# Optimization experiments

Measured on AMD Instinct MI355X. Metric: run time of the kernel, lower is better.

Reference implementation:

```python
import jax, jax.numpy as jnp
import numpy as np

N_NODES = 50000
N_EDGES = 800000
IN_C = 64
HID = 64
OUT_C = 64
N_GRAPHS = 64


def setup_inputs() -> dict:
    key = jax.random.key(0)
    ks = jax.random.split(key, 12)
    x = jax.random.normal(ks[0], (N_NODES, IN_C), dtype=jnp.float32)
    edge_index = jax.random.randint(ks[1], (2, N_EDGES), 0, N_NODES, dtype=jnp.int64)
    # sorted graph-id vector guaranteed to cover all N_GRAPHS segments
    batch = (jnp.arange(N_NODES, dtype=jnp.int64) * N_GRAPHS) // N_NODES
    s = 0.1
    W1_root = jax.random.normal(ks[2], (IN_C, HID), dtype=jnp.float32) * s
    W1_rel = jax.random.normal(ks[3], (IN_C, HID), dtype=jnp.float32) * s
    b1 = jnp.zeros((HID,), dtype=jnp.float32)
    W2_root = jax.random.normal(ks[4], (HID, OUT_C), dtype=jnp.float32) * s
    W2_rel = jax.random.normal(ks[5], (HID, OUT_C), dtype=jnp.float32) * s
    b2 = jnp.zeros((OUT_C,), dtype=jnp.float32)
    fc1_w = jax.random.normal(ks[6], (OUT_C, 8), dtype=jnp.float32) * s
    fc1_b = jnp.zeros((8,), dtype=jnp.float32)
    fc2_w = jax.random.normal(ks[7], (8, 2), dtype=jnp.float32) * s
    fc2_b = jnp.zeros((2,), dtype=jnp.float32)
    return {
        "x": x, "edge_index": edge_index, "batch": batch,
        "W1_root": W1_root, "W1_rel": W1_rel, "b1": b1,
        "W2_root": W2_root, "W2_rel": W2_rel, "b2": b2,
        "fc1_w": fc1_w, "fc1_b": fc1_b, "fc2_w": fc2_w, "fc2_b": fc2_b,
    }


def _graph_conv(h, src, dst, W_root, W_rel, b, n_nodes):
    # PyG GraphConv (aggr='add'): out_i = W_root h_i + W_rel * sum_{j->i} h_j + b
    agg = jax.ops.segment_sum(h[src], dst, num_segments=n_nodes)
    return h @ W_root + agg @ W_rel + b


def reference(x, edge_index, batch, W1_root, W1_rel, b1,
              W2_root, W2_rel, b2, fc1_w, fc1_b, fc2_w, fc2_b):
    n = x.shape[0]
    src, dst = edge_index[0], edge_index[1]
    h = jax.nn.relu(_graph_conv(x, src, dst, W1_root, W1_rel, b1, n))
    h = jax.nn.relu(_graph_conv(h, src, dst, W2_root, W2_rel, b2, n))
    # mid = softmax over first 8 feature columns (split(8,1)[0])
    mid = jax.nn.softmax(h[:, :8], axis=1)
    z = jax.nn.relu(h @ fc1_w + fc1_b)
    z = jax.nn.relu(z @ fc2_w + fc2_b)
    pooled = jax.ops.segment_max(z, batch, num_segments=N_GRAPHS)  # global_max_pool
    out = jax.nn.softmax(pooled, axis=1)
    return (mid, out)
```

## Files before the change

kernel.cpp:

```cpp
#include <hip/hip_runtime.h>
#include <hip/hip_fp16.h>

typedef _Float16 f16_t;
typedef _Float16 f16x8 __attribute__((ext_vector_type(8)));
typedef float f32x4 __attribute__((ext_vector_type(4)));

#define N_NODES 50000
#define N_EDGES 800000
#define C 64
#define N_GRAPHS 64

#define NBKT 782
#define BKT_CAP 1536
#define HS_BLOCKS 256
#define HS_EPB (N_EDGES / HS_BLOCKS)
#define CAST_BLKS 1563
#define CUR_STRIDE 16

#define OFF_CUR    0u
#define OFF_POOLED 51200u
#define OFF_DONE   51712u
#define OFF_EPK    52224u
#define OFF_XH     4857088u
#define OFF_H1H    11257344u
#define OFF_WT1    17657600u
#define OFF_WT2    17673984u

__device__ __forceinline__ unsigned pack2h(float x, float y) {
    __half2 h = __floats2half2_rn(x, y);
    return *reinterpret_cast<unsigned*>(&h);
}

__global__ __launch_bounds__(256) void init_cast_wcast_kernel(
        const float* __restrict__ x, f16_t* __restrict__ xh,
        const float* __restrict__ W1r, const float* __restrict__ W1l, f16_t* __restrict__ Wt1,
        const float* __restrict__ W2r, const float* __restrict__ W2l, f16_t* __restrict__ Wt2,
        int* __restrict__ cur, unsigned int* __restrict__ pooled,
        unsigned int* __restrict__ done_cnt) {
    __shared__ float w0[64 * 64];
    __shared__ float w1[64 * 64];
    const int blk = blockIdx.x;
    const int t = threadIdx.x;
    if (blk < CAST_BLKS) {
        if (blk == 0) {
            for (int i = t; i < NBKT * CUR_STRIDE; i += 256) cur[i] = 0;
            if (t < N_GRAPHS * 2) pooled[t] = 0u;
            if (t == 0) *done_cnt = 0u;
        }
        const int i = blk * 256 + t;
        if (i < N_NODES * C / 8) {
            const float4* p = (const float4*)(x + (size_t)i * 8);
            float4 a = p[0], b = p[1];
            uint4 w;
            w.x = pack2h(a.x, a.y);
            w.y = pack2h(a.z, a.w);
            w.z = pack2h(b.x, b.y);
            w.w = pack2h(b.z, b.w);
            *(uint4*)(xh + (size_t)i * 8) = w;
        }
    } else {
        const int which = blk - CAST_BLKS;
        const float* Wr = which ? W2r : W1r;
        const float* Wl = which ? W2l : W1l;
        f16_t* Wt = which ? Wt2 : Wt1;
        for (int i = t * 4; i < 4096; i += 1024) {
            *(float4*)&w0[i] = *(const float4*)&Wr[i];
            *(float4*)&w1[i] = *(const float4*)&Wl[i];
        }
        __syncthreads();
        const int n = t >> 2, q = t & 3;
        for (int kk = q * 32; kk < q * 32 + 32; kk++) {
            float v = (kk < 64) ? w0[kk * 64 + n] : w1[(kk - 64) * 64 + n];
            Wt[n * 128 + kk] = (f16_t)v;
        }
    }
}

__global__ __launch_bounds__(256) void hist_scatter_kernel(const int* __restrict__ src,
                                                           const int* __restrict__ dst,
                                                           int* __restrict__ cur,
                                                           int* __restrict__ epk) {
    __shared__ int h[NBKT];
    __shared__ int base_s[NBKT];
    const int t = threadIdx.x;
    const int blk = blockIdx.x;
    for (int i = t; i < NBKT; i += 256) h[i] = 0;
    __syncthreads();
    const int beg = blk * HS_EPB;
    for (int i = beg + t; i < beg + HS_EPB; i += 256)
        atomicAdd(&h[dst[i] >> 6], 1);
    __syncthreads();
    for (int b = t; b < NBKT; b += 256) {
        int hv = h[b];
        int old = hv ? atomicAdd(&cur[b * CUR_STRIDE], hv) : 0;
        base_s[b] = b * BKT_CAP + old;
        h[b] = 0;
    }
    __syncthreads();
    for (int i = beg + t; i < beg + HS_EPB; i += 256) {
        int d = dst[i];
        int b = d >> 6;
        int off = atomicAdd(&h[b], 1);
        int pos = base_s[b] + off;
        if (pos < (b + 1) * BKT_CAP)
            epk[pos] = src[i] | ((d & 63) << 16);
    }
}

__device__ __forceinline__ void agg_stage_mfma(
        const f16_t* __restrict__ Hsrc,
        const int* __restrict__ epk_blk, int n_edges,
        const f16_t* __restrict__ Wt, const float* __restrict__ bias,
        f16_t* Als, f16_t* Wls, int* eb, int* cnt, int* beg,
        int row0, int t, f32x4& acc, int& ncol, int& outrow0) {
    const int cr = t >> 4, cj = t & 15;
    int gxr = row0 + cr; if (gxr > N_NODES - 1) gxr = N_NODES - 1;
    uint2 xv = *(const uint2*)(Hsrc + (size_t)gxr * 64 + cj * 4);
    uint4 wvv = *(const uint4*)(Wt + cr * 128 + cj * 8);
    if (t < 64) cnt[t] = 0;
    __syncthreads();
    int pk0 = (t < n_edges) ? epk_blk[t] : -1;
    int pk1 = (t + 1024 < n_edges) ? epk_blk[t + 1024] : -1;
    if (pk0 >= 0) atomicAdd(&cnt[pk0 >> 16], 1);
    if (pk1 >= 0) atomicAdd(&cnt[pk1 >> 16], 1);
    __syncthreads();
    if (t < 64) {
        int v = cnt[t];
        int ex = v;
        #pragma unroll
        for (int d = 1; d < 64; d <<= 1) {
            int o = __shfl_up(ex, d);
            if (t >= d) ex += o;
        }
        beg[t] = ex - v;
        cnt[t] = ex - v;
    }
    __syncthreads();
    if (pk0 >= 0) eb[atomicAdd(&cnt[pk0 >> 16], 1)] = pk0 & 0xFFFF;
    if (pk1 >= 0) eb[atomicAdd(&cnt[pk1 >> 16], 1)] = pk1 & 0xFFFF;
    __syncthreads();
    const int wv = t >> 6, lane = t & 63;
    const int slot = lane >> 4, j = lane & 15;
    const uint2* hw = (const uint2*)Hsrc;
    #pragma unroll
    for (int i = 0; i < 4; i++) {
        const int dl = wv * 4 + i;
        const int b0 = beg[dl], e1 = cnt[dl];
        float s0 = 0.f, s1 = 0.f, s2 = 0.f, s3 = 0.f;
        int e = b0;
        for (; e + 16 <= e1; e += 16) {
            int i0 = eb[e + slot];
            int i1 = eb[e + 4 + slot];
            int i2 = eb[e + 8 + slot];
            int i3 = eb[e + 12 + slot];
            uint2 u0 = hw[(size_t)i0 * 16 + j];
            uint2 u1 = hw[(size_t)i1 * 16 + j];
            uint2 u2 = hw[(size_t)i2 * 16 + j];
            uint2 u3 = hw[(size_t)i3 * 16 + j];
            float2 a, b;
            a = __half22float2(*(__half2*)&u0.x); b = __half22float2(*(__half2*)&u0.y);
            s0 += a.x; s1 += a.y; s2 += b.x; s3 += b.y;
            a = __half22float2(*(__half2*)&u1.x); b = __half22float2(*(__half2*)&u1.y);
            s0 += a.x; s1 += a.y; s2 += b.x; s3 += b.y;
            a = __half22float2(*(__half2*)&u2.x); b = __half22float2(*(__half2*)&u2.y);
            s0 += a.x; s1 += a.y; s2 += b.x; s3 += b.y;
            a = __half22float2(*(__half2*)&u3.x); b = __half22float2(*(__half2*)&u3.y);
            s0 += a.x; s1 += a.y; s2 += b.x; s3 += b.y;
        }
        for (; e + 4 <= e1; e += 4) {
            int i0 = eb[e + slot];
            uint2 u = hw[(size_t)i0 * 16 + j];
            float2 a = __half22float2(*(__half2*)&u.x);
            float2 b = __half22float2(*(__half2*)&u.y);
            s0 += a.x; s1 += a.y; s2 += b.x; s3 += b.y;
        }
        int rem = e1 - e;
        if (slot < rem) {
            int i0 = eb[e + slot];
            uint2 u = hw[(size_t)i0 * 16 + j];
            float2 a = __half22float2(*(__half2*)&u.x);
            float2 b = __half22float2(*(__half2*)&u.y);
            s0 += a.x; s1 += a.y; s2 += b.x; s3 += b.y;
        }
        s0 += __shfl_xor(s0, 16); s1 += __shfl_xor(s1, 16);
        s2 += __shfl_xor(s2, 16); s3 += __shfl_xor(s3, 16);
        s0 += __shfl_xor(s0, 32); s1 += __shfl_xor(s1, 32);
        s2 += __shfl_xor(s2, 32); s3 += __shfl_xor(s3, 32);
        if (slot == 0) {
            uint2 o; o.x = pack2h(s0, s1); o.y = pack2h(s2, s3);
            *(uint2*)((char*)Als + dl * 256 + ((128 + j * 8) ^ ((dl & 7) << 4))) = o;
        }
    }
    *(uint2*)((char*)Als + cr * 256 + ((cj * 8) ^ ((cr & 7) << 4))) = xv;
    *(uint4*)((char*)Wls + cr * 256 + ((cj * 16) ^ ((cr & 7) << 4))) = wvv;
    __syncthreads();
    const int lr = lane & 15, kh = lane >> 4;
    const int wr = wv >> 2, wc = wv & 3;
    const int arow = wr * 16 + lr;
    ncol = wc * 16 + lr;
    outrow0 = row0 + wr * 16 + kh * 4;
    float bv = bias[ncol];
    acc = (f32x4){bv, bv, bv, bv};
    #pragma unroll
    for (int kt = 0; kt < 4; kt++) {
        const int kb = (kt * 32 + kh * 8) * 2;
        f16x8 a = *(const f16x8*)((const char*)Als + arow * 256 + (kb ^ ((arow & 7) << 4)));
        f16x8 b = *(const f16x8*)((const char*)Wls + ncol * 256 + (kb ^ ((ncol & 7) << 4)));
        acc = __builtin_amdgcn_mfma_f32_16x16x32_f16(a, b, acc, 0, 0, 0);
    }
}

__global__ __launch_bounds__(1024) void layer1_kernel(const f16_t* __restrict__ xh,
                                                      const int* __restrict__ epk,
                                                      const int* __restrict__ cur,
                                                      const f16_t* __restrict__ Wt,
                                                      const float* __restrict__ bias,
                                                      f16_t* __restrict__ h1h) {
    __shared__ f16_t Als[64 * 128];
    __shared__ f16_t Wls[64 * 128];
    __shared__ int eb[BKT_CAP];
    __shared__ int cnt[64];
    __shared__ int beg[64];
    const int t = threadIdx.x;
    const int blk = blockIdx.x;
    const int row0 = blk * 64;
    int n = cur[blk * CUR_STRIDE]; if (n > BKT_CAP) n = BKT_CAP;
    f32x4 acc; int ncol, outrow0;
    agg_stage_mfma(xh, epk + (size_t)blk * BKT_CAP, n, Wt, bias,
                   Als, Wls, eb, cnt, beg, row0, t, acc, ncol, outrow0);
    #pragma unroll
    for (int rr = 0; rr < 4; rr++) {
        const int gm = outrow0 + rr;
        if (gm < N_NODES)
            h1h[(size_t)gm * 64 + ncol] = (f16_t)fmaxf(acc[rr], 0.f);
    }
}

__global__ __launch_bounds__(1024) void layer2_head_kernel(
        const f16_t* __restrict__ h1h,
        const int* __restrict__ epk, const int* __restrict__ cur,
        const f16_t* __restrict__ Wt, const float* __restrict__ bias,
        const int* __restrict__ batch,
        const float* __restrict__ fc1w, const float* __restrict__ fc1b,
        const float* __restrict__ fc2w, const float* __restrict__ fc2b,
        float* __restrict__ mid_out, unsigned int* __restrict__ pooled,
        unsigned int* __restrict__ done_cnt, float* __restrict__ fin_out) {
    __shared__ f16_t Als[64 * 128];
    __shared__ f16_t Wls[64 * 128];
    __shared__ int eb[BKT_CAP];
    __shared__ int cnt[64];
    __shared__ int beg[64];
    __shared__ float tile[64 * 65];
    __shared__ float w1s[512];
    __shared__ float z1s[64 * 9];
    __shared__ float b1s[8];
    __shared__ float w2s[16];
    __shared__ float b2s[2];
    __shared__ unsigned int pool_s[N_GRAPHS * 2];
    __shared__ unsigned int amLast;
    __shared__ float fin[N_GRAPHS * 2];
    const int t = threadIdx.x;
    const int blk = blockIdx.x;
    const int row0 = blk * 64;
    if (t < 512) w1s[t] = fc1w[t];
    if (t >= 512 && t < 520) b1s[t - 512] = fc1b[t - 512];
    if (t >= 520 && t < 536) w2s[t - 520] = fc2w[t - 520];
    if (t >= 536 && t < 538) b2s[t - 536] = fc2b[t - 536];
    if (t >= 544 && t < 544 + N_GRAPHS * 2) pool_s[t - 544] = 0u;
    int n = cur[blk * CUR_STRIDE]; if (n > BKT_CAP) n = BKT_CAP;
    f32x4 acc; int ncol, outrow0;
    agg_stage_mfma(h1h, epk + (size_t)blk * BKT_CAP, n, Wt, bias,
                   Als, Wls, eb, cnt, beg, row0, t, acc, ncol, outrow0);
    #pragma unroll
    for (int rr = 0; rr < 4; rr++)
        tile[(outrow0 - row0 + rr) * 65 + ncol] = fmaxf(acc[rr], 0.f);
    __syncthreads();
    const int row = t & 63, qq = t >> 6;
    const int gm = row0 + row;
    const bool valid = gm < N_NODES;
    if (qq < 4) {
        float z0 = b1s[2 * qq], z1v = b1s[2 * qq + 1];
        for (int k = 0; k < 64; k++) {
            float a = tile[row * 65 + k];
            z0  += a * w1s[k * 8 + 2 * qq];
            z1v += a * w1s[k * 8 + 2 * qq + 1];
        }
        z1s[row * 9 + 2 * qq]     = fmaxf(z0, 0.f);
        z1s[row * 9 + 2 * qq + 1] = fmaxf(z1v, 0.f);
    }
    if (qq == 4 && valid) {
        float rv[8];
        #pragma unroll
        for (int c = 0; c < 8; c++) rv[c] = tile[row * 65 + c];
        float m = rv[0];
        #pragma unroll
        for (int c = 1; c < 8; c++) m = fmaxf(m, rv[c]);
        float ex[8], s = 0.f;
        #pragma unroll
        for (int c = 0; c < 8; c++) { ex[c] = __expf(rv[c] - m); s += ex[c]; }
        float inv = 1.f / s;
        float4 v0 = {ex[0] * inv, ex[1] * inv, ex[2] * inv, ex[3] * inv};
        float4 v1 = {ex[4] * inv, ex[5] * inv, ex[6] * inv, ex[7] * inv};
        *(float4*)&mid_out[(size_t)gm * 8]     = v0;
        *(float4*)&mid_out[(size_t)gm * 8 + 4] = v1;
    }
    __syncthreads();
    if (qq == 0 && valid) {
        float z20 = b2s[0], z21 = b2s[1];
        #pragma unroll
        for (int o = 0; o < 8; o++) {
            float z = z1s[row * 9 + o];
            z20 += z * w2s[o * 2];
            z21 += z * w2s[o * 2 + 1];
        }
        z20 = fmaxf(z20, 0.f);
        z21 = fmaxf(z21, 0.f);
        int b = batch[gm];
        atomicMax(&pool_s[b * 2 + 0], __float_as_uint(z20));
        atomicMax(&pool_s[b * 2 + 1], __float_as_uint(z21));
    }
    __syncthreads();
    if (t < N_GRAPHS * 2) {
        unsigned int v = pool_s[t];
        if (v) atomicMax(&pooled[t], v);
    }
    __syncthreads();
    if (t == 0) {
        __threadfence();
        unsigned int prev = atomicAdd(done_cnt, 1u);
        amLast = (prev == gridDim.x - 1) ? 1u : 0u;
    }
    __syncthreads();
    if (amLast) {
        if (t < N_GRAPHS * 2) fin[t] = __uint_as_float(atomicMax(&pooled[t], 0u));
        __syncthreads();
        if (t < N_GRAPHS) {
            float v0 = fin[2 * t], v1 = fin[2 * t + 1];
            float m = fmaxf(v0, v1);
            float e0 = __expf(v0 - m), e1 = __expf(v1 - m);
            float s = e0 + e1;
            fin_out[2 * t]     = e0 / s;
            fin_out[2 * t + 1] = e1 / s;
        }
    }
}

extern "C" void kernel_launch(void* const* d_in, const int* in_sizes, int n_in,
                              void* d_out, int out_size, void* d_ws, size_t ws_size,
                              hipStream_t stream) {
    const float* x    = (const float*)d_in[0];
    const int*   ei   = (const int*)d_in[1];
    const int*   batch= (const int*)d_in[2];
    const float* W1r  = (const float*)d_in[3];
    const float* W1l  = (const float*)d_in[4];
    const float* b1   = (const float*)d_in[5];
    const float* W2r  = (const float*)d_in[6];
    const float* W2l  = (const float*)d_in[7];
    const float* b2   = (const float*)d_in[8];
    const float* fc1w = (const float*)d_in[9];
    const float* fc1b = (const float*)d_in[10];
    const float* fc2w = (const float*)d_in[11];
    const float* fc2b = (const float*)d_in[12];

    const int* src = ei;
    const int* dst = ei + N_EDGES;

    char* ws = (char*)d_ws;
    int*    cur    = (int*)(ws + OFF_CUR);
    unsigned int* pooled   = (unsigned int*)(ws + OFF_POOLED);
    unsigned int* done_cnt = (unsigned int*)(ws + OFF_DONE);
    int*    epk    = (int*)(ws + OFF_EPK);
    f16_t*  xh     = (f16_t*)(ws + OFF_XH);
    f16_t*  h1h    = (f16_t*)(ws + OFF_H1H);
    f16_t*  Wt1    = (f16_t*)(ws + OFF_WT1);
    f16_t*  Wt2    = (f16_t*)(ws + OFF_WT2);

    float* mid_out = (float*)d_out;
    float* fin_out = (float*)d_out + (size_t)N_NODES * 8;

    init_cast_wcast_kernel<<<CAST_BLKS + 2, 256, 0, stream>>>(
        x, xh, W1r, W1l, Wt1, W2r, W2l, Wt2, cur, pooled, done_cnt);
    hist_scatter_kernel<<<HS_BLOCKS, 256, 0, stream>>>(src, dst, cur, epk);

    layer1_kernel<<<NBKT, 1024, 0, stream>>>(xh, epk, cur, Wt1, b1, h1h);
    layer2_head_kernel<<<NBKT, 1024, 0, stream>>>(h1h, epk, cur, Wt2, b2, batch,
                                                  fc1w, fc1b, fc2w, fc2b,
                                                  mid_out, pooled, done_cnt, fin_out);
}
```

Before: 96.83 us.

## Halve node bucket size to 32 rows with 512-thread blocks and shared-memory aliasing

```diff
diff --git a/kernel.cpp b/kernel.cpp
--- a/kernel.cpp
+++ b/kernel.cpp
@@ -10,21 +10,21 @@
 #define C 64
 #define N_GRAPHS 64
 
-#define NBKT 782
-#define BKT_CAP 1536
+#define NBKT 1563
+#define BKT_CAP 768
 #define HS_BLOCKS 256
 #define HS_EPB (N_EDGES / HS_BLOCKS)
 #define CAST_BLKS 1563
 #define CUR_STRIDE 16
 
 #define OFF_CUR    0u
-#define OFF_POOLED 51200u
-#define OFF_DONE   51712u
-#define OFF_EPK    52224u
-#define OFF_XH     4857088u
-#define OFF_H1H    11257344u
-#define OFF_WT1    17657600u
-#define OFF_WT2    17673984u
+#define OFF_POOLED 100096u
+#define OFF_DONE   100608u
+#define OFF_EPK    101120u
+#define OFF_XH     4903680u
+#define OFF_H1H    11303936u
+#define OFF_WT1    17704192u
+#define OFF_WT2    17720576u
 
 __device__ __forceinline__ unsigned pack2h(float x, float y) {
     __half2 h = __floats2half2_rn(x, y);
@@ -88,7 +88,7 @@
     __syncthreads();
     const int beg = blk * HS_EPB;
     for (int i = beg + t; i < beg + HS_EPB; i += 256)
-        atomicAdd(&h[dst[i] >> 6], 1);
+        atomicAdd(&h[dst[i] >> 5], 1);
     __syncthreads();
     for (int b = t; b < NBKT; b += 256) {
         int hv = h[b];
@@ -99,11 +99,11 @@
     __syncthreads();
     for (int i = beg + t; i < beg + HS_EPB; i += 256) {
         int d = dst[i];
-        int b = d >> 6;
+        int b = d >> 5;
         int off = atomicAdd(&h[b], 1);
         int pos = base_s[b] + off;
         if (pos < (b + 1) * BKT_CAP)
-            epk[pos] = src[i] | ((d & 63) << 16);
+            epk[pos] = src[i] | ((d & 31) << 16);
     }
 }
 
@@ -116,19 +116,21 @@
     const int cr = t >> 4, cj = t & 15;
     int gxr = row0 + cr; if (gxr > N_NODES - 1) gxr = N_NODES - 1;
     uint2 xv = *(const uint2*)(Hsrc + (size_t)gxr * 64 + cj * 4);
-    uint4 wvv = *(const uint4*)(Wt + cr * 128 + cj * 8);
-    if (t < 64) cnt[t] = 0;
+    const int wn = t >> 3, wc8 = t & 7;
+    uint4 wv0 = *(const uint4*)(Wt + wn * 128 + wc8 * 8);
+    uint4 wv1 = *(const uint4*)(Wt + wn * 128 + (wc8 + 8) * 8);
+    if (t < 32) cnt[t] = 0;
     __syncthreads();
     int pk0 = (t < n_edges) ? epk_blk[t] : -1;
-    int pk1 = (t + 1024 < n_edges) ? epk_blk[t + 1024] : -1;
+    int pk1 = (t + 512 < n_edges) ? epk_blk[t + 512] : -1;
     if (pk0 >= 0) atomicAdd(&cnt[pk0 >> 16], 1);
     if (pk1 >= 0) atomicAdd(&cnt[pk1 >> 16], 1);
     __syncthreads();
-    if (t < 64) {
+    if (t < 32) {
         int v = cnt[t];
         int ex = v;
         #pragma unroll
-        for (int d = 1; d < 64; d <<= 1) {
+        for (int d = 1; d < 32; d <<= 1) {
             int o = __shfl_up(ex, d);
             if (t >= d) ex += o;
         }
@@ -192,7 +194,8 @@
         }
     }
     *(uint2*)((char*)Als + cr * 256 + ((cj * 8) ^ ((cr & 7) << 4))) = xv;
-    *(uint4*)((char*)Wls + cr * 256 + ((cj * 16) ^ ((cr & 7) << 4))) = wvv;
+    *(uint4*)((char*)Wls + wn * 256 + ((wc8 * 16) ^ ((wn & 7) << 4))) = wv0;
+    *(uint4*)((char*)Wls + wn * 256 + (((wc8 + 8) * 16) ^ ((wn & 7) << 4))) = wv1;
     __syncthreads();
     const int lr = lane & 15, kh = lane >> 4;
     const int wr = wv >> 2, wc = wv & 3;
@@ -210,20 +213,20 @@
     }
 }
 
-__global__ __launch_bounds__(1024) void layer1_kernel(const f16_t* __restrict__ xh,
-                                                      const int* __restrict__ epk,
-                                                      const int* __restrict__ cur,
-                                                      const f16_t* __restrict__ Wt,
-                                                      const float* __restrict__ bias,
-                                                      f16_t* __restrict__ h1h) {
-    __shared__ f16_t Als[64 * 128];
+__global__ __launch_bounds__(512, 8) void layer1_kernel(const f16_t* __restrict__ xh,
+                                                        const int* __restrict__ epk,
+                                                        const int* __restrict__ cur,
+                                                        const f16_t* __restrict__ Wt,
+                                                        const float* __restrict__ bias,
+                                                        f16_t* __restrict__ h1h) {
+    __shared__ f16_t Als[32 * 128];
     __shared__ f16_t Wls[64 * 128];
     __shared__ int eb[BKT_CAP];
-    __shared__ int cnt[64];
-    __shared__ int beg[64];
+    __shared__ int cnt[32];
+    __shared__ int beg[32];
     const int t = threadIdx.x;
     const int blk = blockIdx.x;
-    const int row0 = blk * 64;
+    const int row0 = blk * 32;
     int n = cur[blk * CUR_STRIDE]; if (n > BKT_CAP) n = BKT_CAP;
     f32x4 acc; int ncol, outrow0;
     agg_stage_mfma(xh, epk + (size_t)blk * BKT_CAP, n, Wt, bias,
@@ -236,7 +239,7 @@
     }
 }
 
-__global__ __launch_bounds__(1024) void layer2_head_kernel(
+__global__ __launch_bounds__(512, 8) void layer2_head_kernel(
         const f16_t* __restrict__ h1h,
         const int* __restrict__ epk, const int* __restrict__ cur,
         const f16_t* __restrict__ Wt, const float* __restrict__ bias,
@@ -245,37 +248,39 @@
         const float* __restrict__ fc2w, const float* __restrict__ fc2b,
         float* __restrict__ mid_out, unsigned int* __restrict__ pooled,
         unsigned int* __restrict__ done_cnt, float* __restrict__ fin_out) {
-    __shared__ f16_t Als[64 * 128];
+    __shared__ __align__(16) char smem[11520];
     __shared__ f16_t Wls[64 * 128];
-    __shared__ int eb[BKT_CAP];
-    __shared__ int cnt[64];
-    __shared__ int beg[64];
-    __shared__ float tile[64 * 65];
     __shared__ float w1s[512];
-    __shared__ float z1s[64 * 9];
+    __shared__ float z1s[32 * 9];
     __shared__ float b1s[8];
     __shared__ float w2s[16];
     __shared__ float b2s[2];
     __shared__ unsigned int pool_s[N_GRAPHS * 2];
     __shared__ unsigned int amLast;
     __shared__ float fin[N_GRAPHS * 2];
+    f16_t* Als = (f16_t*)smem;
+    int*   eb  = (int*)(smem + 8192);
+    int*   cnt = (int*)(smem + 11264);
+    int*   beg = (int*)(smem + 11392);
+    float* tile = (float*)smem;
     const int t = threadIdx.x;
     const int blk = blockIdx.x;
-    const int row0 = blk * 64;
+    const int row0 = blk * 32;
     if (t < 512) w1s[t] = fc1w[t];
-    if (t >= 512 && t < 520) b1s[t - 512] = fc1b[t - 512];
-    if (t >= 520 && t < 536) w2s[t - 520] = fc2w[t - 520];
-    if (t >= 536 && t < 538) b2s[t - 536] = fc2b[t - 536];
-    if (t >= 544 && t < 544 + N_GRAPHS * 2) pool_s[t - 544] = 0u;
+    if (t < 8) b1s[t] = fc1b[t];
+    if (t < 16) w2s[t] = fc2w[t];
+    if (t < 2) b2s[t] = fc2b[t];
+    if (t < N_GRAPHS * 2) pool_s[t] = 0u;
     int n = cur[blk * CUR_STRIDE]; if (n > BKT_CAP) n = BKT_CAP;
     f32x4 acc; int ncol, outrow0;
     agg_stage_mfma(h1h, epk + (size_t)blk * BKT_CAP, n, Wt, bias,
                    Als, Wls, eb, cnt, beg, row0, t, acc, ncol, outrow0);
+    __syncthreads();
     #pragma unroll
     for (int rr = 0; rr < 4; rr++)
         tile[(outrow0 - row0 + rr) * 65 + ncol] = fmaxf(acc[rr], 0.f);
     __syncthreads();
-    const int row = t & 63, qq = t >> 6;
+    const int row = t & 31, qq = t >> 5;
     const int gm = row0 + row;
     const bool valid = gm < N_NODES;
     if (qq < 4) {
@@ -382,8 +387,8 @@
         x, xh, W1r, W1l, Wt1, W2r, W2l, Wt2, cur, pooled, done_cnt);
     hist_scatter_kernel<<<HS_BLOCKS, 256, 0, stream>>>(src, dst, cur, epk);
 
-    layer1_kernel<<<NBKT, 1024, 0, stream>>>(xh, epk, cur, Wt1, b1, h1h);
-    layer2_head_kernel<<<NBKT, 1024, 0, stream>>>(h1h, epk, cur, Wt2, b2, batch,
-                                                  fc1w, fc1b, fc2w, fc2b,
-                                                  mid_out, pooled, done_cnt, fin_out);
-}
+    layer1_kernel<<<NBKT, 512, 0, stream>>>(xh, epk, cur, Wt1, b1, h1h);
+    layer2_head_kernel<<<NBKT, 512, 0, stream>>>(h1h, epk, cur, Wt2, b2, batch,
+                                                 fc1w, fc1b, fc2w, fc2b,
+                                                 mid_out, pooled, done_cnt, fin_out);
+}
```

After: 116.4 us. 20.2% more time.

## Split fp16 feature tables into two 32-column halves for gather locality

Applied to the files above, without the earlier changes.

```diff
diff --git a/kernel.cpp b/kernel.cpp
--- a/kernel.cpp
+++ b/kernel.cpp
@@ -21,10 +21,12 @@
 #define OFF_POOLED 51200u
 #define OFF_DONE   51712u
 #define OFF_EPK    52224u
-#define OFF_XH     4857088u
-#define OFF_H1H    11257344u
-#define OFF_WT1    17657600u
-#define OFF_WT2    17673984u
+#define OFF_XLO    4857088u
+#define OFF_XHI    8057344u
+#define OFF_H1LO   11257600u
+#define OFF_H1HI   14457856u
+#define OFF_WT1    17658112u
+#define OFF_WT2    17674496u
 
 __device__ __forceinline__ unsigned pack2h(float x, float y) {
     __half2 h = __floats2half2_rn(x, y);
@@ -32,7 +34,7 @@
 }
 
 __global__ __launch_bounds__(256) void init_cast_wcast_kernel(
-        const float* __restrict__ x, f16_t* __restrict__ xh,
+        const float* __restrict__ x, f16_t* __restrict__ xlo, f16_t* __restrict__ xhi,
         const float* __restrict__ W1r, const float* __restrict__ W1l, f16_t* __restrict__ Wt1,
         const float* __restrict__ W2r, const float* __restrict__ W2l, f16_t* __restrict__ Wt2,
         int* __restrict__ cur, unsigned int* __restrict__ pooled,
@@ -49,6 +51,7 @@
         }
         const int i = blk * 256 + t;
         if (i < N_NODES * C / 8) {
+            const int n = i >> 3, f0 = (i & 7) * 8;
             const float4* p = (const float4*)(x + (size_t)i * 8);
             float4 a = p[0], b = p[1];
             uint4 w;
@@ -56,7 +59,9 @@
             w.y = pack2h(a.z, a.w);
             w.z = pack2h(b.x, b.y);
             w.w = pack2h(b.z, b.w);
-            *(uint4*)(xh + (size_t)i * 8) = w;
+            f16_t* dst = (f0 < 32) ? (xlo + (size_t)n * 32 + f0)
+                                   : (xhi + (size_t)n * 32 + (f0 - 32));
+            *(uint4*)dst = w;
         }
     } else {
         const int which = blk - CAST_BLKS;
@@ -108,14 +113,16 @@
 }
 
 __device__ __forceinline__ void agg_stage_mfma(
-        const f16_t* __restrict__ Hsrc,
+        const f16_t* __restrict__ Hlo, const f16_t* __restrict__ Hhi,
         const int* __restrict__ epk_blk, int n_edges,
         const f16_t* __restrict__ Wt, const float* __restrict__ bias,
         f16_t* Als, f16_t* Wls, int* eb, int* cnt, int* beg,
         int row0, int t, f32x4& acc, int& ncol, int& outrow0) {
     const int cr = t >> 4, cj = t & 15;
     int gxr = row0 + cr; if (gxr > N_NODES - 1) gxr = N_NODES - 1;
-    uint2 xv = *(const uint2*)(Hsrc + (size_t)gxr * 64 + cj * 4);
+    uint2 xv = (cj < 8)
+        ? *(const uint2*)(Hlo + (size_t)gxr * 32 + cj * 4)
+        : *(const uint2*)(Hhi + (size_t)gxr * 32 + (cj - 8) * 4);
     uint4 wvv = *(const uint4*)(Wt + cr * 128 + cj * 8);
     if (t < 64) cnt[t] = 0;
     __syncthreads();
@@ -140,55 +147,74 @@
     if (pk1 >= 0) eb[atomicAdd(&cnt[pk1 >> 16], 1)] = pk1 & 0xFFFF;
     __syncthreads();
     const int wv = t >> 6, lane = t & 63;
-    const int slot = lane >> 4, j = lane & 15;
-    const uint2* hw = (const uint2*)Hsrc;
+    const int slot = lane >> 3, j = lane & 7;
     #pragma unroll
-    for (int i = 0; i < 4; i++) {
-        const int dl = wv * 4 + i;
-        const int b0 = beg[dl], e1 = cnt[dl];
-        float s0 = 0.f, s1 = 0.f, s2 = 0.f, s3 = 0.f;
-        int e = b0;
-        for (; e + 16 <= e1; e += 16) {
-            int i0 = eb[e + slot];
-            int i1 = eb[e + 4 + slot];
-            int i2 = eb[e + 8 + slot];
-            int i3 = eb[e + 12 + slot];
-            uint2 u0 = hw[(size_t)i0 * 16 + j];
-            uint2 u1 = hw[(size_t)i1 * 16 + j];
-            uint2 u2 = hw[(size_t)i2 * 16 + j];
-            uint2 u3 = hw[(size_t)i3 * 16 + j];
-            float2 a, b;
-            a = __half22float2(*(__half2*)&u0.x); b = __half22float2(*(__half2*)&u0.y);
-            s0 += a.x; s1 += a.y; s2 += b.x; s3 += b.y;
-            a = __half22float2(*(__half2*)&u1.x); b = __half22float2(*(__half2*)&u1.y);
-            s0 += a.x; s1 += a.y; s2 += b.x; s3 += b.y;
-            a = __half22float2(*(__half2*)&u2.x); b = __half22float2(*(__half2*)&u2.y);
-            s0 += a.x; s1 += a.y; s2 += b.x; s3 += b.y;
-            a = __half22float2(*(__half2*)&u3.x); b = __half22float2(*(__half2*)&u3.y);
-            s0 += a.x; s1 += a.y; s2 += b.x; s3 += b.y;
-        }
-        for (; e + 4 <= e1; e += 4) {
-            int i0 = eb[e + slot];
-            uint2 u = hw[(size_t)i0 * 16 + j];
-            float2 a = __half22float2(*(__half2*)&u.x);
-            float2 b = __half22float2(*(__half2*)&u.y);
-            s0 += a.x; s1 += a.y; s2 += b.x; s3 += b.y;
-        }
-        int rem = e1 - e;
-        if (slot < rem) {
-            int i0 = eb[e + slot];
-            uint2 u = hw[(size_t)i0 * 16 + j];
-            float2 a = __half22float2(*(__half2*)&u.x);
-            float2 b = __half22float2(*(__half2*)&u.y);
-            s0 += a.x; s1 += a.y; s2 += b.x; s3 += b.y;
-        }
-        s0 += __shfl_xor(s0, 16); s1 += __shfl_xor(s1, 16);
-        s2 += __shfl_xor(s2, 16); s3 += __shfl_xor(s3, 16);
-        s0 += __shfl_xor(s0, 32); s1 += __shfl_xor(s1, 32);
-        s2 += __shfl_xor(s2, 32); s3 += __shfl_xor(s3, 32);
-        if (slot == 0) {
-            uint2 o; o.x = pack2h(s0, s1); o.y = pack2h(s2, s3);
-            *(uint2*)((char*)Als + dl * 256 + ((128 + j * 8) ^ ((dl & 7) << 4))) = o;
+    for (int hsel = 0; hsel < 2; hsel++) {
+        const uint2* hw = (const uint2*)(hsel ? Hhi : Hlo);
+        #pragma unroll
+        for (int i = 0; i < 4; i++) {
+            const int dl = wv * 4 + i;
+            const int b0 = beg[dl], e1 = cnt[dl];
+            float s0 = 0.f, s1 = 0.f, s2 = 0.f, s3 = 0.f;
+            int e = b0;
+            for (; e + 32 <= e1; e += 32) {
+                int i0 = eb[e + slot];
+                int i1 = eb[e + 8 + slot];
+                int i2 = eb[e + 16 + slot];
+                int i3 = eb[e + 24 + slot];
+                uint2 u0 = hw[(size_t)i0 * 8 + j];
+                uint2 u1 = hw[(size_t)i1 * 8 + j];
+                uint2 u2 = hw[(size_t)i2 * 8 + j];
+                uint2 u3 = hw[(size_t)i3 * 8 + j];
+                float2 a, b;
+                a = __half22float2(*(__half2*)&u0.x); b = __half22float2(*(__half2*)&u0.y);
+                s0 += a.x; s1 += a.y; s2 += b.x; s3 += b.y;
+                a = __half22float2(*(__half2*)&u1.x); b = __half22float2(*(__half2*)&u1.y);
+                s0 += a.x; s1 += a.y; s2 += b.x; s3 += b.y;
+                a = __half22float2(*(__half2*)&u2.x); b = __half22float2(*(__half2*)&u2.y);
+                s0 += a.x; s1 += a.y; s2 += b.x; s3 += b.y;
+                a = __half22float2(*(__half2*)&u3.x); b = __half22float2(*(__half2*)&u3.y);
+                s0 += a.x; s1 += a.y; s2 += b.x; s3 += b.y;
+            }
+            if (e + 16 <= e1) {
+                int i0 = eb[e + slot];
+                int i1 = eb[e + 8 + slot];
+                uint2 u0 = hw[(size_t)i0 * 8 + j];
+                uint2 u1 = hw[(size_t)i1 * 8 + j];
+                float2 a, b;
+                a = __half22float2(*(__half2*)&u0.x); b = __half22float2(*(__half2*)&u0.y);
+                s0 += a.x; s1 += a.y; s2 += b.x; s3 += b.y;
+                a = __half22float2(*(__half2*)&u1.x); b = __half22float2(*(__half2*)&u1.y);
+                s0 += a.x; s1 += a.y; s2 += b.x; s3 += b.y;
+                e += 16;
+            }
+            if (e + 8 <= e1) {
+                int i0 = eb[e + slot];
+                uint2 u = hw[(size_t)i0 * 8 + j];
+                float2 a = __half22float2(*(__half2*)&u.x);
+                float2 b = __half22float2(*(__half2*)&u.y);
+                s0 += a.x; s1 += a.y; s2 += b.x; s3 += b.y;
+                e += 8;
+            }
+            int rem = e1 - e;
+            if (slot < rem) {
+                int i0 = eb[e + slot];
+                uint2 u = hw[(size_t)i0 * 8 + j];
+                float2 a = __half22float2(*(__half2*)&u.x);
+                float2 b = __half22float2(*(__half2*)&u.y);
+                s0 += a.x; s1 += a.y; s2 += b.x; s3 += b.y;
+            }
+            s0 += __shfl_xor(s0, 8);  s1 += __shfl_xor(s1, 8);
+            s2 += __shfl_xor(s2, 8);  s3 += __shfl_xor(s3, 8);
+            s0 += __shfl_xor(s0, 16); s1 += __shfl_xor(s1, 16);
+            s2 += __shfl_xor(s2, 16); s3 += __shfl_xor(s3, 16);
+            s0 += __shfl_xor(s0, 32); s1 += __shfl_xor(s1, 32);
+            s2 += __shfl_xor(s2, 32); s3 += __shfl_xor(s3, 32);
+            if (slot == 0) {
+                uint2 o; o.x = pack2h(s0, s1); o.y = pack2h(s2, s3);
+                *(uint2*)((char*)Als + dl * 256 +
+                          ((128 + hsel * 64 + j * 8) ^ ((dl & 7) << 4))) = o;
+            }
         }
     }
     *(uint2*)((char*)Als + cr * 256 + ((cj * 8) ^ ((cr & 7) << 4))) = xv;
@@ -210,12 +236,14 @@
     }
 }
 
-__global__ __launch_bounds__(1024) void layer1_kernel(const f16_t* __restrict__ xh,
+__global__ __launch_bounds__(1024) void layer1_kernel(const f16_t* __restrict__ xlo,
+                                                      const f16_t* __restrict__ xhi,
                                                       const int* __restrict__ epk,
                                                       const int* __restrict__ cur,
                                                       const f16_t* __restrict__ Wt,
                                                       const float* __restrict__ bias,
-                                                      f16_t* __restrict__ h1h) {
+                                                      f16_t* __restrict__ h1lo,
+                                                      f16_t* __restrict__ h1hi) {
     __shared__ f16_t Als[64 * 128];
     __shared__ f16_t Wls[64 * 128];
     __shared__ int eb[BKT_CAP];
@@ -226,18 +254,20 @@
     const int row0 = blk * 64;
     int n = cur[blk * CUR_STRIDE]; if (n > BKT_CAP) n = BKT_CAP;
     f32x4 acc; int ncol, outrow0;
-    agg_stage_mfma(xh, epk + (size_t)blk * BKT_CAP, n, Wt, bias,
+    agg_stage_mfma(xlo, xhi, epk + (size_t)blk * BKT_CAP, n, Wt, bias,
                    Als, Wls, eb, cnt, beg, row0, t, acc, ncol, outrow0);
+    f16_t* outp = (ncol < 32) ? h1lo : h1hi;
+    const int oc = ncol & 31;
     #pragma unroll
     for (int rr = 0; rr < 4; rr++) {
         const int gm = outrow0 + rr;
         if (gm < N_NODES)
-            h1h[(size_t)gm * 64 + ncol] = (f16_t)fmaxf(acc[rr], 0.f);
+            outp[(size_t)gm * 32 + oc] = (f16_t)fmaxf(acc[rr], 0.f);
     }
 }
 
 __global__ __launch_bounds__(1024) void layer2_head_kernel(
-        const f16_t* __restrict__ h1h,
+        const f16_t* __restrict__ h1lo, const f16_t* __restrict__ h1hi,
         const int* __restrict__ epk, const int* __restrict__ cur,
         const f16_t* __restrict__ Wt, const float* __restrict__ bias,
         const int* __restrict__ batch,
@@ -269,7 +299,7 @@
     if (t >= 544 && t < 544 + N_GRAPHS * 2) pool_s[t - 544] = 0u;
     int n = cur[blk * CUR_STRIDE]; if (n > BKT_CAP) n = BKT_CAP;
     f32x4 acc; int ncol, outrow0;
-    agg_stage_mfma(h1h, epk + (size_t)blk * BKT_CAP, n, Wt, bias,
+    agg_stage_mfma(h1lo, h1hi, epk + (size_t)blk * BKT_CAP, n, Wt, bias,
                    Als, Wls, eb, cnt, beg, row0, t, acc, ncol, outrow0);
     #pragma unroll
     for (int rr = 0; rr < 4; rr++)
@@ -370,8 +400,10 @@
     unsigned int* pooled   = (unsigned int*)(ws + OFF_POOLED);
     unsigned int* done_cnt = (unsigned int*)(ws + OFF_DONE);
     int*    epk    = (int*)(ws + OFF_EPK);
-    f16_t*  xh     = (f16_t*)(ws + OFF_XH);
-    f16_t*  h1h    = (f16_t*)(ws + OFF_H1H);
+    f16_t*  xlo    = (f16_t*)(ws + OFF_XLO);
+    f16_t*  xhi    = (f16_t*)(ws + OFF_XHI);
+    f16_t*  h1lo   = (f16_t*)(ws + OFF_H1LO);
+    f16_t*  h1hi   = (f16_t*)(ws + OFF_H1HI);
     f16_t*  Wt1    = (f16_t*)(ws + OFF_WT1);
     f16_t*  Wt2    = (f16_t*)(ws + OFF_WT2);
 
@@ -379,11 +411,12 @@
     float* fin_out = (float*)d_out + (size_t)N_NODES * 8;
 
     init_cast_wcast_kernel<<<CAST_BLKS + 2, 256, 0, stream>>>(
-        x, xh, W1r, W1l, Wt1, W2r, W2l, Wt2, cur, pooled, done_cnt);
+        x, xlo, xhi, W1r, W1l, Wt1, W2r, W2l, Wt2, cur, pooled, done_cnt);
     hist_scatter_kernel<<<HS_BLOCKS, 256, 0, stream>>>(src, dst, cur, epk);
 
-    layer1_kernel<<<NBKT, 1024, 0, stream>>>(xh, epk, cur, Wt1, b1, h1h);
-    layer2_head_kernel<<<NBKT, 1024, 0, stream>>>(h1h, epk, cur, Wt2, b2, batch,
-                                                  fc1w, fc1b, fc2w, fc2b,
+    layer1_kernel<<<NBKT, 1024, 0, stream>>>(xlo, xhi, epk, cur, Wt1, b1,
+                                             h1lo, h1hi);
+    layer2_head_kernel<<<NBKT, 1024, 0, stream>>>(h1lo, h1hi, epk, cur, Wt2, b2,
+                                                  batch, fc1w, fc1b, fc2w, fc2b,
                                                   mid_out, pooled, done_cnt, fin_out);
 }
```

Result: slower. 120.2 us (+24.1%).
